# Optimization experiments

Hardware: AMD Instinct MI355X
Metric: run time of the kernel (lower is better)

## Reference

```python
import jax, jax.numpy as jnp
import numpy as np

N_NODES = 100000
N_EDGES = 1600000
NODE_DIM = 5
HIDDEN = 64
N_LAYERS = 3


def setup_inputs() -> dict:
    key = jax.random.key(0)
    ks = jax.random.split(key, 12)
    s = 0.1
    return {
        "x": jax.random.normal(ks[0], (N_NODES, NODE_DIM), dtype=jnp.float32),
        "edge_index": jax.random.randint(ks[1], (2, N_EDGES), 0, N_NODES, dtype=jnp.int32),
        # message MLP params per layer (stacked over layers)
        "W1": jax.random.normal(ks[2], (N_LAYERS, 2 * NODE_DIM, HIDDEN), dtype=jnp.float32) * s,
        "b1": jnp.zeros((N_LAYERS, HIDDEN), dtype=jnp.float32),
        "W2": jax.random.normal(ks[3], (N_LAYERS, HIDDEN, NODE_DIM), dtype=jnp.float32) * s,
        "b2": jnp.zeros((N_LAYERS, NODE_DIM), dtype=jnp.float32),
        # update MLP params per layer
        "U1": jax.random.normal(ks[4], (N_LAYERS, 2 * NODE_DIM, HIDDEN), dtype=jnp.float32) * s,
        "bu1": jnp.zeros((N_LAYERS, HIDDEN), dtype=jnp.float32),
        "U2": jax.random.normal(ks[5], (N_LAYERS, HIDDEN, NODE_DIM), dtype=jnp.float32) * s,
        "bu2": jnp.zeros((N_LAYERS, NODE_DIM), dtype=jnp.float32),
        # readout
        "Wr": jax.random.normal(ks[6], (NODE_DIM, NODE_DIM), dtype=jnp.float32) * s,
        "br": jnp.zeros((NODE_DIM,), dtype=jnp.float32),
    }


def reference(x, edge_index, W1, b1, W2, b2, U1, bu1, U2, bu2, Wr, br):
    # PyG convention: messages flow from source j = edge_index[0] to target i = edge_index[1]
    src = edge_index[0]
    dst = edge_index[1]
    n = x.shape[0]
    for l in range(N_LAYERS):
        x_i = x[dst]                                   # [E, d] target features
        x_j = x[src]                                   # [E, d] source features
        msg_in = jnp.concatenate([x_i, x_j], axis=-1)  # [E, 2d]
        msg = jax.nn.relu(msg_in @ W1[l] + b1[l]) @ W2[l] + b2[l]   # [E, d]
        aggr = jax.ops.segment_sum(msg, dst, num_segments=n)        # [N, d] scatter-add at targets
        upd_in = jnp.concatenate([x, aggr], axis=-1)   # [N, 2d]
        upd = jax.nn.relu(upd_in @ U1[l] + bu1[l]) @ U2[l] + bu2[l]  # [N, d]
        x = upd + x                                    # residual (in SkeletonGNN.forward)
    return x @ Wr + br
```

## Files before the change

kernel.cpp:

```cpp
#include <hip/hip_runtime.h>

#define N_NODES 100000
#define N_EDGES 1600000
#define DIM 5
#define HID 64
#define N_LAYERS 3
#define SCAN_BLK 256
#define NBLK ((N_NODES + SCAN_BLK - 1) / SCAN_BLK)

__global__ __launch_bounds__(256) void fused_hist_msg1_kernel(
    const float* __restrict__ x,
    const int* __restrict__ ei,
    const float* __restrict__ W1, const float* __restrict__ b1,
    const float* __restrict__ W2, const float* __restrict__ b2,
    int* __restrict__ cnt, int* __restrict__ rank,
    float* __restrict__ msg0)
{
    int e = blockIdx.x * blockDim.x + threadIdx.x;
    if (e >= N_EDGES) return;
    int src = ei[e];
    int dst = ei[N_EDGES + e];

    int rk = atomicAdd(&cnt[dst], 1);

    float in[10];
    const float* xi = x + (long)dst * DIM;
    const float* xj = x + (long)src * DIM;
#pragma unroll
    for (int d = 0; d < DIM; ++d) in[d] = xi[d];
#pragma unroll
    for (int d = 0; d < DIM; ++d) in[DIM + d] = xj[d];

    float msg[DIM];
#pragma unroll
    for (int j = 0; j < DIM; ++j) msg[j] = b2[j];

#pragma unroll 8
    for (int h = 0; h < HID; ++h) {
        float acc = b1[h];
#pragma unroll
        for (int d = 0; d < 10; ++d) acc = fmaf(in[d], W1[d * HID + h], acc);
        acc = fmaxf(acc, 0.0f);
#pragma unroll
        for (int j = 0; j < DIM; ++j) msg[j] = fmaf(acc, W2[h * DIM + j], msg[j]);
    }

    float* mp = msg0 + (long)e * DIM;
#pragma unroll
    for (int j = 0; j < DIM; ++j) mp[j] = msg[j];

    rank[e] = rk;
}


__global__ __launch_bounds__(SCAN_BLK) void scan_part_kernel(
    const int* __restrict__ cnt, int* __restrict__ blk_sum)
{
    __shared__ int s[SCAN_BLK];
    int t = threadIdx.x;
    int i = blockIdx.x * SCAN_BLK + t;
    s[t] = (i < N_NODES) ? cnt[i] : 0;
    __syncthreads();
    for (int off = SCAN_BLK / 2; off > 0; off >>= 1) {
        if (t < off) s[t] += s[t + off];
        __syncthreads();
    }
    if (t == 0) blk_sum[blockIdx.x] = s[0];
}

__global__ __launch_bounds__(512) void scan_blk_kernel(
    const int* __restrict__ blk_sum, int* __restrict__ blk_pref)
{
    __shared__ int s[512];
    int t = threadIdx.x;
    int v = (t < NBLK) ? blk_sum[t] : 0;
    s[t] = v;
    __syncthreads();
    for (int off = 1; off < 512; off <<= 1) {
        int a = (t >= off) ? s[t - off] : 0;
        __syncthreads();
        s[t] += a;
        __syncthreads();
    }
    if (t < NBLK) blk_pref[t] = s[t] - v;
}

__global__ __launch_bounds__(SCAN_BLK) void scan_add_kernel(
    const int* __restrict__ cnt, const int* __restrict__ blk_pref,
    int* __restrict__ row_ptr)
{
    __shared__ int s[SCAN_BLK];
    int t = threadIdx.x;
    int i = blockIdx.x * SCAN_BLK + t;
    int c = (i < N_NODES) ? cnt[i] : 0;
    s[t] = c;
    __syncthreads();
    for (int off = 1; off < SCAN_BLK; off <<= 1) {
        int a = (t >= off) ? s[t - off] : 0;
        __syncthreads();
        s[t] += a;
        __syncthreads();
    }
    if (i < N_NODES) row_ptr[i] = blk_pref[blockIdx.x] + s[t] - c;
    if (i == 0) row_ptr[N_NODES] = N_EDGES;
}

__global__ __launch_bounds__(256) void scatter_pair_perm_kernel(
    const int* __restrict__ ei, const int* __restrict__ rank,
    const int* __restrict__ row_ptr,
    int2* __restrict__ spair, int* __restrict__ eperm)
{
    int e = blockIdx.x * blockDim.x + threadIdx.x;
    if (e >= N_EDGES) return;
    int src = ei[e];
    int dst = ei[N_EDGES + e];
    int pos = row_ptr[dst] + rank[e];
    spair[pos] = make_int2(src, dst);
    eperm[pos] = e;
}


__global__ __launch_bounds__(256) void edge_msg_sorted_kernel(
    const float* __restrict__ x,
    const int2* __restrict__ spair,
    const float* __restrict__ W1, const float* __restrict__ b1,
    const float* __restrict__ W2, const float* __restrict__ b2,
    float* __restrict__ msg_buf)
{
    int e = blockIdx.x * blockDim.x + threadIdx.x;
    if (e >= N_EDGES) return;
    int2 p = spair[e];

    float in[10];
    const float* xi = x + (long)p.y * DIM;
    const float* xj = x + (long)p.x * DIM;
#pragma unroll
    for (int d = 0; d < DIM; ++d) in[d] = xi[d];
#pragma unroll
    for (int d = 0; d < DIM; ++d) in[DIM + d] = xj[d];

    float msg[DIM];
#pragma unroll
    for (int j = 0; j < DIM; ++j) msg[j] = b2[j];

#pragma unroll 8
    for (int h = 0; h < HID; ++h) {
        float acc = b1[h];
#pragma unroll
        for (int d = 0; d < 10; ++d) acc = fmaf(in[d], W1[d * HID + h], acc);
        acc = fmaxf(acc, 0.0f);
#pragma unroll
        for (int j = 0; j < DIM; ++j) msg[j] = fmaf(acc, W2[h * DIM + j], msg[j]);
    }

    float* mp = msg_buf + (long)e * DIM;
#pragma unroll
    for (int j = 0; j < DIM; ++j) mp[j] = msg[j];
}

template <bool FINAL, bool INDIRECT>
__global__ __launch_bounds__(256) void gather_update8_kernel(
    const float* __restrict__ x,
    const float* __restrict__ msg_buf,
    const int* __restrict__ eperm,
    const int* __restrict__ row_ptr,
    const float* __restrict__ U1, const float* __restrict__ bu1,
    const float* __restrict__ U2, const float* __restrict__ bu2,
    const float* __restrict__ Wr, const float* __restrict__ br,
    float* __restrict__ xout)
{
    int gt = blockIdx.x * blockDim.x + threadIdx.x;
    int v = gt >> 3;
    int r = gt & 7;
    if (v >= N_NODES) return;

    int s = row_ptr[v], e1 = row_ptr[v + 1];

    float agg[DIM] = {0.f, 0.f, 0.f, 0.f, 0.f};
    for (int e = s + r; e < e1; e += 8) {
        long me = INDIRECT ? (long)eperm[e] : (long)e;
        const float* mp = msg_buf + me * DIM;
#pragma unroll
        for (int j = 0; j < DIM; ++j) agg[j] += mp[j];
    }
#pragma unroll
    for (int m = 1; m < 8; m <<= 1) {
#pragma unroll
        for (int j = 0; j < DIM; ++j) agg[j] += __shfl_xor(agg[j], m, 64);
    }

    float in2[10];
#pragma unroll
    for (int d = 0; d < DIM; ++d) in2[d] = x[(long)v * DIM + d];
#pragma unroll
    for (int d = 0; d < DIM; ++d) in2[DIM + d] = agg[d];

    float upd[DIM] = {0.f, 0.f, 0.f, 0.f, 0.f};
#pragma unroll
    for (int hh = 0; hh < 8; ++hh) {
        int h = r + hh * 8;
        float acc = bu1[h];
#pragma unroll
        for (int d = 0; d < 10; ++d) acc = fmaf(in2[d], U1[d * HID + h], acc);
        acc = fmaxf(acc, 0.0f);
#pragma unroll
        for (int j = 0; j < DIM; ++j) upd[j] = fmaf(acc, U2[h * DIM + j], upd[j]);
    }
#pragma unroll
    for (int m = 1; m < 8; m <<= 1) {
#pragma unroll
        for (int j = 0; j < DIM; ++j) upd[j] += __shfl_xor(upd[j], m, 64);
    }

    if (r == 0) {
        float xn[DIM];
#pragma unroll
        for (int j = 0; j < DIM; ++j) xn[j] = upd[j] + bu2[j] + in2[j];
        if (FINAL) {
#pragma unroll
            for (int j = 0; j < DIM; ++j) {
                float o = br[j];
#pragma unroll
                for (int d = 0; d < DIM; ++d) o = fmaf(xn[d], Wr[d * DIM + j], o);
                xout[(long)v * DIM + j] = o;
            }
        } else {
#pragma unroll
            for (int j = 0; j < DIM; ++j) xout[(long)v * DIM + j] = xn[j];
        }
    }
}


__global__ __launch_bounds__(256) void edge_msg_kernel(
    const float* __restrict__ x, const int* __restrict__ ei,
    const float* __restrict__ W1, const float* __restrict__ b1,
    const float* __restrict__ W2, const float* __restrict__ b2,
    float* __restrict__ aggr)
{
    int e = blockIdx.x * blockDim.x + threadIdx.x;
    if (e >= N_EDGES) return;
    int src = ei[e];
    int dst = ei[N_EDGES + e];
    float in[10];
    const float* xi = x + (long)dst * DIM;
    const float* xj = x + (long)src * DIM;
#pragma unroll
    for (int d = 0; d < DIM; ++d) in[d] = xi[d];
#pragma unroll
    for (int d = 0; d < DIM; ++d) in[DIM + d] = xj[d];
    float msg[DIM];
#pragma unroll
    for (int j = 0; j < DIM; ++j) msg[j] = b2[j];
#pragma unroll 8
    for (int h = 0; h < HID; ++h) {
        float acc = b1[h];
#pragma unroll
        for (int d = 0; d < 10; ++d) acc = fmaf(in[d], W1[d * HID + h], acc);
        acc = fmaxf(acc, 0.0f);
#pragma unroll
        for (int j = 0; j < DIM; ++j) msg[j] = fmaf(acc, W2[h * DIM + j], msg[j]);
    }
    float* ap = aggr + (long)dst * DIM;
#pragma unroll
    for (int j = 0; j < DIM; ++j) atomicAdd(ap + j, msg[j]);
}

template <bool FINAL>
__global__ __launch_bounds__(256) void node_upd_kernel(
    const float* __restrict__ x, const float* __restrict__ aggr,
    const float* __restrict__ U1, const float* __restrict__ bu1,
    const float* __restrict__ U2, const float* __restrict__ bu2,
    const float* __restrict__ Wr, const float* __restrict__ br,
    float* __restrict__ xout)
{
    int v = blockIdx.x * blockDim.x + threadIdx.x;
    if (v >= N_NODES) return;
    float in[10];
#pragma unroll
    for (int d = 0; d < DIM; ++d) in[d] = x[(long)v * DIM + d];
#pragma unroll
    for (int d = 0; d < DIM; ++d) in[DIM + d] = aggr[(long)v * DIM + d];
    float upd[DIM];
#pragma unroll
    for (int j = 0; j < DIM; ++j) upd[j] = bu2[j];
#pragma unroll 8
    for (int h = 0; h < HID; ++h) {
        float acc = bu1[h];
#pragma unroll
        for (int d = 0; d < 10; ++d) acc = fmaf(in[d], U1[d * HID + h], acc);
        acc = fmaxf(acc, 0.0f);
#pragma unroll
        for (int j = 0; j < DIM; ++j) upd[j] = fmaf(acc, U2[h * DIM + j], upd[j]);
    }
    float xn[DIM];
#pragma unroll
    for (int j = 0; j < DIM; ++j) xn[j] = upd[j] + in[j];
    if (FINAL) {
#pragma unroll
        for (int j = 0; j < DIM; ++j) {
            float o = br[j];
#pragma unroll
            for (int d = 0; d < DIM; ++d) o = fmaf(xn[d], Wr[d * DIM + j], o);
            xout[(long)v * DIM + j] = o;
        }
    } else {
#pragma unroll
        for (int j = 0; j < DIM; ++j) xout[(long)v * DIM + j] = xn[j];
    }
}


static inline size_t alignup(size_t x) { return (x + 255) & ~(size_t)255; }

extern "C" void kernel_launch(void* const* d_in, const int* in_sizes, int n_in,
                              void* d_out, int out_size, void* d_ws, size_t ws_size,
                              hipStream_t stream) {
    const float* x   = (const float*)d_in[0];
    const int*   ei  = (const int*)d_in[1];
    const float* W1  = (const float*)d_in[2];
    const float* b1  = (const float*)d_in[3];
    const float* W2  = (const float*)d_in[4];
    const float* b2  = (const float*)d_in[5];
    const float* U1  = (const float*)d_in[6];
    const float* bu1 = (const float*)d_in[7];
    const float* U2  = (const float*)d_in[8];
    const float* bu2 = (const float*)d_in[9];
    const float* Wr  = (const float*)d_in[10];
    const float* br  = (const float*)d_in[11];
    float* out = (float*)d_out;

    char* ws = (char*)d_ws;

    size_t o_cnt  = 0;
    size_t o_row  = alignup(o_cnt + (size_t)N_NODES * 4);
    size_t o_bsum = alignup(o_row + (size_t)(N_NODES + 1) * 4);
    size_t o_bpre = alignup(o_bsum + (size_t)NBLK * 4);
    size_t o_sp   = alignup(o_bpre + (size_t)NBLK * 4);
    size_t o_perm = alignup(o_sp + (size_t)N_EDGES * 8);
    size_t o_rank = alignup(o_perm + (size_t)N_EDGES * 4);
    size_t o_xA   = alignup(o_rank + (size_t)N_EDGES * 4);
    size_t o_xB   = alignup(o_xA + (size_t)N_NODES * DIM * 4);
    size_t o_msg  = alignup(o_xB + (size_t)N_NODES * DIM * 4);
    size_t needed = o_msg + (size_t)N_EDGES * DIM * 4;

    dim3 blk(256);
    dim3 eg((N_EDGES + 255) / 256);
    dim3 ng((N_NODES + 255) / 256);
    dim3 ng8((N_NODES * 8 + 255) / 256);

    if (ws_size < needed) {
        size_t nbytes = (size_t)N_NODES * DIM * sizeof(float);
        float* aggr = (float*)ws;
        float* xA   = (float*)(ws + nbytes);
        float* xB   = (float*)(ws + 2 * nbytes);
        const float* xcur = x;
        for (int l = 0; l < N_LAYERS; ++l) {
            hipMemsetAsync(aggr, 0, nbytes, stream);
            edge_msg_kernel<<<eg, blk, 0, stream>>>(
                xcur, ei, W1 + l * 10 * HID, b1 + l * HID,
                W2 + l * HID * DIM, b2 + l * DIM, aggr);
            if (l < N_LAYERS - 1) {
                float* xn = (l == 0) ? xA : xB;
                node_upd_kernel<false><<<ng, blk, 0, stream>>>(
                    xcur, aggr, U1 + l * 10 * HID, bu1 + l * HID,
                    U2 + l * HID * DIM, bu2 + l * DIM, Wr, br, xn);
                xcur = xn;
            } else {
                node_upd_kernel<true><<<ng, blk, 0, stream>>>(
                    xcur, aggr, U1 + l * 10 * HID, bu1 + l * HID,
                    U2 + l * HID * DIM, bu2 + l * DIM, Wr, br, out);
            }
        }
        return;
    }

    int* cnt      = (int*)(ws + o_cnt);
    int* row_ptr  = (int*)(ws + o_row);
    int* blk_sum  = (int*)(ws + o_bsum);
    int* blk_pref = (int*)(ws + o_bpre);
    int2* spair   = (int2*)(ws + o_sp);
    int* eperm    = (int*)(ws + o_perm);
    int* rank     = (int*)(ws + o_rank);
    float* xA     = (float*)(ws + o_xA);
    float* xB     = (float*)(ws + o_xB);
    float* msgbuf = (float*)(ws + o_msg);

    hipMemsetAsync(cnt, 0, (size_t)N_NODES * 4, stream);
    fused_hist_msg1_kernel<<<eg, blk, 0, stream>>>(
        x, ei, W1, b1, W2, b2, cnt, rank, msgbuf);

    scan_part_kernel<<<NBLK, SCAN_BLK, 0, stream>>>(cnt, blk_sum);
    scan_blk_kernel<<<1, 512, 0, stream>>>(blk_sum, blk_pref);
    scan_add_kernel<<<NBLK, SCAN_BLK, 0, stream>>>(cnt, blk_pref, row_ptr);
    scatter_pair_perm_kernel<<<eg, blk, 0, stream>>>(ei, rank, row_ptr, spair, eperm);

    gather_update8_kernel<false, true><<<ng8, blk, 0, stream>>>(
        x, msgbuf, eperm, row_ptr, U1, bu1, U2, bu2, Wr, br, xA);

    edge_msg_sorted_kernel<<<eg, blk, 0, stream>>>(
        xA, spair, W1 + 10 * HID, b1 + HID,
        W2 + HID * DIM, b2 + DIM, msgbuf);
    gather_update8_kernel<false, false><<<ng8, blk, 0, stream>>>(
        xA, msgbuf, nullptr, row_ptr, U1 + 10 * HID, bu1 + HID,
        U2 + HID * DIM, bu2 + DIM, Wr, br, xB);

    edge_msg_sorted_kernel<<<eg, blk, 0, stream>>>(
        xB, spair, W1 + 2 * 10 * HID, b1 + 2 * HID,
        W2 + 2 * HID * DIM, b2 + 2 * DIM, msgbuf);
    gather_update8_kernel<true, false><<<ng8, blk, 0, stream>>>(
        xB, msgbuf, nullptr, row_ptr, U1 + 2 * 10 * HID, bu1 + 2 * HID,
        U2 + 2 * HID * DIM, bu2 + 2 * DIM, Wr, br, out);
}
```

Measured before the change: 388.1 us.

## Fuse edge message computation with in-block segmented reduction into node aggregates

For layers 2 and 3, the edge message kernel now reduces messages for runs of equal destination inside each 256-edge block through shared memory. Interior runs are written directly and runs at block boundaries are atomically added into a zeroed aggregate buffer. This removes the per-edge message buffer round trip and the CSR gather in the update kernel. It adds a memset per layer, atomics at block edges and a serial per-run loop in shared memory, which can be unbalanced for high-degree nodes.

```diff
diff --git a/kernel.cpp b/kernel.cpp
--- a/kernel.cpp
+++ b/kernel.cpp
@@ -119,43 +119,129 @@
     eperm[pos] = e;
 }
 
-
-__global__ __launch_bounds__(256) void edge_msg_sorted_kernel(
+__global__ __launch_bounds__(256) void edge_msg_reduce_kernel(
     const float* __restrict__ x,
     const int2* __restrict__ spair,
     const float* __restrict__ W1, const float* __restrict__ b1,
     const float* __restrict__ W2, const float* __restrict__ b2,
-    float* __restrict__ msg_buf)
-{
-    int e = blockIdx.x * blockDim.x + threadIdx.x;
-    if (e >= N_EDGES) return;
-    int2 p = spair[e];
-
-    float in[10];
-    const float* xi = x + (long)p.y * DIM;
-    const float* xj = x + (long)p.x * DIM;
-#pragma unroll
-    for (int d = 0; d < DIM; ++d) in[d] = xi[d];
-#pragma unroll
-    for (int d = 0; d < DIM; ++d) in[DIM + d] = xj[d];
-
-    float msg[DIM];
-#pragma unroll
-    for (int j = 0; j < DIM; ++j) msg[j] = b2[j];
-
+    float* __restrict__ aggr)
+{
+    __shared__ float lmsg[256][DIM];
+    __shared__ int ldst[256];
+
+    int tid = threadIdx.x;
+    int e0 = blockIdx.x * 256;
+    int bsize = N_EDGES - e0;
+    if (bsize > 256) bsize = 256;
+    bool active = tid < bsize;
+
+    int src = 0, dst = -1;
+    if (active) {
+        int2 p = spair[e0 + tid];
+        src = p.x; dst = p.y;
+    }
+    ldst[tid] = dst;
+
+    float msg[DIM] = {0.f, 0.f, 0.f, 0.f, 0.f};
+    if (active) {
+        float in[10];
+        const float* xi = x + (long)dst * DIM;
+        const float* xj = x + (long)src * DIM;
+#pragma unroll
+        for (int d = 0; d < DIM; ++d) in[d] = xi[d];
+#pragma unroll
+        for (int d = 0; d < DIM; ++d) in[DIM + d] = xj[d];
+#pragma unroll
+        for (int j = 0; j < DIM; ++j) msg[j] = b2[j];
 #pragma unroll 8
-    for (int h = 0; h < HID; ++h) {
-        float acc = b1[h];
-#pragma unroll
-        for (int d = 0; d < 10; ++d) acc = fmaf(in[d], W1[d * HID + h], acc);
+        for (int h = 0; h < HID; ++h) {
+            float acc = b1[h];
+#pragma unroll
+            for (int d = 0; d < 10; ++d) acc = fmaf(in[d], W1[d * HID + h], acc);
+            acc = fmaxf(acc, 0.0f);
+#pragma unroll
+            for (int j = 0; j < DIM; ++j) msg[j] = fmaf(acc, W2[h * DIM + j], msg[j]);
+        }
+    }
+#pragma unroll
+    for (int j = 0; j < DIM; ++j) lmsg[tid][j] = msg[j];
+    __syncthreads();
+
+    if (active && (tid == 0 || ldst[tid - 1] != dst)) {
+        float acc[DIM];
+#pragma unroll
+        for (int j = 0; j < DIM; ++j) acc[j] = msg[j];
+        int i = tid + 1;
+        while (i < bsize && ldst[i] == dst) {
+#pragma unroll
+            for (int j = 0; j < DIM; ++j) acc[j] += lmsg[i][j];
+            ++i;
+        }
+        float* ap = aggr + (long)dst * DIM;
+        if (tid == 0 || i == bsize) {
+#pragma unroll
+            for (int j = 0; j < DIM; ++j) atomicAdd(ap + j, acc[j]);
+        } else {
+#pragma unroll
+            for (int j = 0; j < DIM; ++j) ap[j] = acc[j];
+        }
+    }
+}
+
+template <bool FINAL>
+__global__ __launch_bounds__(256) void node_upd8_kernel(
+    const float* __restrict__ x,
+    const float* __restrict__ aggr,
+    const float* __restrict__ U1, const float* __restrict__ bu1,
+    const float* __restrict__ U2, const float* __restrict__ bu2,
+    const float* __restrict__ Wr, const float* __restrict__ br,
+    float* __restrict__ xout)
+{
+    int gt = blockIdx.x * blockDim.x + threadIdx.x;
+    int v = gt >> 3;
+    int r = gt & 7;
+    if (v >= N_NODES) return;
+
+    float in2[10];
+#pragma unroll
+    for (int d = 0; d < DIM; ++d) in2[d] = x[(long)v * DIM + d];
+#pragma unroll
+    for (int d = 0; d < DIM; ++d) in2[DIM + d] = aggr[(long)v * DIM + d];
+
+    float upd[DIM] = {0.f, 0.f, 0.f, 0.f, 0.f};
+#pragma unroll
+    for (int hh = 0; hh < 8; ++hh) {
+        int h = r + hh * 8;
+        float acc = bu1[h];
+#pragma unroll
+        for (int d = 0; d < 10; ++d) acc = fmaf(in2[d], U1[d * HID + h], acc);
         acc = fmaxf(acc, 0.0f);
 #pragma unroll
-        for (int j = 0; j < DIM; ++j) msg[j] = fmaf(acc, W2[h * DIM + j], msg[j]);
-    }
-
-    float* mp = msg_buf + (long)e * DIM;
-#pragma unroll
-    for (int j = 0; j < DIM; ++j) mp[j] = msg[j];
+        for (int j = 0; j < DIM; ++j) upd[j] = fmaf(acc, U2[h * DIM + j], upd[j]);
+    }
+#pragma unroll
+    for (int m = 1; m < 8; m <<= 1) {
+#pragma unroll
+        for (int j = 0; j < DIM; ++j) upd[j] += __shfl_xor(upd[j], m, 64);
+    }
+
+    if (r == 0) {
+        float xn[DIM];
+#pragma unroll
+        for (int j = 0; j < DIM; ++j) xn[j] = upd[j] + bu2[j] + in2[j];
+        if (FINAL) {
+#pragma unroll
+            for (int j = 0; j < DIM; ++j) {
+                float o = br[j];
+#pragma unroll
+                for (int d = 0; d < DIM; ++d) o = fmaf(xn[d], Wr[d * DIM + j], o);
+                xout[(long)v * DIM + j] = o;
+            }
+        } else {
+#pragma unroll
+            for (int j = 0; j < DIM; ++j) xout[(long)v * DIM + j] = xn[j];
+        }
+    }
 }
 
 template <bool FINAL, bool INDIRECT>
@@ -385,6 +471,7 @@
     float* xA     = (float*)(ws + o_xA);
     float* xB     = (float*)(ws + o_xB);
     float* msgbuf = (float*)(ws + o_msg);
+    float* aggr   = (float*)(ws + o_msg);
 
     hipMemsetAsync(cnt, 0, (size_t)N_NODES * 4, stream);
     fused_hist_msg1_kernel<<<eg, blk, 0, stream>>>(
@@ -398,17 +485,18 @@
     gather_update8_kernel<false, true><<<ng8, blk, 0, stream>>>(
         x, msgbuf, eperm, row_ptr, U1, bu1, U2, bu2, Wr, br, xA);
 
-    edge_msg_sorted_kernel<<<eg, blk, 0, stream>>>(
-        xA, spair, W1 + 10 * HID, b1 + HID,
-        W2 + HID * DIM, b2 + DIM, msgbuf);
-    gather_update8_kernel<false, false><<<ng8, blk, 0, stream>>>(
-        xA, msgbuf, nullptr, row_ptr, U1 + 10 * HID, bu1 + HID,
+    hipMemsetAsync(aggr, 0, (size_t)N_NODES * DIM * 4, stream);
+    edge_msg_reduce_kernel<<<eg, blk, 0, stream>>>(
+        xA, spair, W1 + 10 * HID, b1 + HID, W2 + HID * DIM, b2 + DIM, aggr);
+    node_upd8_kernel<false><<<ng8, blk, 0, stream>>>(
+        xA, aggr, U1 + 10 * HID, bu1 + HID,
         U2 + HID * DIM, bu2 + DIM, Wr, br, xB);
 
-    edge_msg_sorted_kernel<<<eg, blk, 0, stream>>>(
+    hipMemsetAsync(aggr, 0, (size_t)N_NODES * DIM * 4, stream);
+    edge_msg_reduce_kernel<<<eg, blk, 0, stream>>>(
         xB, spair, W1 + 2 * 10 * HID, b1 + 2 * HID,
-        W2 + 2 * HID * DIM, b2 + 2 * DIM, msgbuf);
-    gather_update8_kernel<true, false><<<ng8, blk, 0, stream>>>(
-        xB, msgbuf, nullptr, row_ptr, U1 + 2 * 10 * HID, bu1 + 2 * HID,
+        W2 + 2 * HID * DIM, b2 + 2 * DIM, aggr);
+    node_upd8_kernel<true><<<ng8, blk, 0, stream>>>(
+        xB, aggr, U1 + 2 * 10 * HID, bu1 + 2 * HID,
         U2 + 2 * HID * DIM, bu2 + 2 * DIM, Wr, br, out);
 }
```

Result: slower. 401.2 us (+3.4%).
